# Performance work log

Measured on AMD Instinct MI355X. Metric: run time of the kernel, lower is better.

Reference implementation:

```python
import jax, jax.numpy as jnp
import numpy as np

B, R, K, C, H, E = 256, 6, 49, 512, 1024, 300
NV, NR, NL = 504, 190, 2001


def setup_inputs() -> dict:
    key = jax.random.key(0)
    ks = list(jax.random.split(key, 40))
    it = iter(ks)

    def nrm(shape, s=0.02):
        return jax.random.normal(next(it), shape, jnp.float32) * s

    return dict(
        v_org=jax.random.normal(next(it), (B, C, 7, 7), jnp.float32),
        img_feat=jax.random.normal(next(it), (B, K, C), jnp.float32),
        gt_verb=jax.random.randint(next(it), (B,), 0, NV),
        role_idx=jax.random.randint(next(it), (B, R), 0, NR),
        mask=jnp.ones((B, R, R), jnp.int32),
        verb_table=nrm((NV, E)),
        role_table=nrm((NR, E)),
        qc_W=nrm((2 * E, H)), qc_b=jnp.zeros((H,), jnp.float32),
        av_W=nrm((C, H)), av_b=jnp.zeros((H,), jnp.float32),
        aq_W=nrm((H, H)), aq_b=jnp.zeros((H,), jnp.float32),
        ao_W=nrm((H, 1)), ao_b=jnp.zeros((1,), jnp.float32),
        vn_W=nrm((C, H)), vn_b=jnp.zeros((H,), jnp.float32),
        qn_W=nrm((H, H)), qn_b=jnp.zeros((H,), jnp.float32),
        Wq=nrm((H, H)), Wk=nrm((H, H)), Wv=nrm((H, H)), Wo=nrm((H, H)),
        uqc_W=nrm((H + 2 * E, H)), uqc_b=jnp.zeros((H,), jnp.float32),
        cls_W=nrm((H, NL)), cls_b=jnp.zeros((NL,), jnp.float32),
    )


def _mfb(q_repr, v_repr):
    # elementwise MFB pool (n_heads=1 -> sumpool is identity), sign-sqrt, L2 norm
    z = q_repr * v_repr
    s = jnp.sqrt(jax.nn.relu(z)) - jnp.sqrt(jax.nn.relu(-z))
    n = jnp.sqrt(jnp.sum(s * s, axis=1, keepdims=True))
    return s / jnp.maximum(n, 1e-12)


def _v_att(img, q_emb, av_W, av_b, aq_W, aq_b, ao_W, ao_b):
    v = jax.nn.relu(img @ av_W + av_b)            # [N,K,H]
    q = jax.nn.relu(q_emb @ aq_W + aq_b)          # [N,H]
    logits = (v * q[:, None, :]) @ ao_W + ao_b    # [N,K,1]
    return jax.nn.softmax(logits, axis=1)


def reference(v_org, img_feat, gt_verb, role_idx, mask, verb_table, role_table,
              qc_W, qc_b, av_W, av_b, aq_W, aq_b, ao_W, ao_b,
              vn_W, vn_b, qn_W, qn_b, Wq, Wk, Wv, Wo,
              uqc_W, uqc_b, cls_W, cls_b):
    Bn, Cn, h, w = v_org.shape
    Rn = role_idx.shape[1]
    img0 = v_org.reshape(Bn, Cn, h * w).transpose(0, 2, 1)          # [B,K,C]
    img = jnp.broadcast_to(img0[:, None], (Bn, Rn, h * w, Cn)).reshape(Bn * Rn, h * w, Cn)
    Kv, Cv = img_feat.shape[1], img_feat.shape[2]
    img_v = jnp.broadcast_to(img_feat[:, None], (Bn, Rn, Kv, Cv)).reshape(Bn * Rn, Kv, Cv)

    verb_e = verb_table[gt_verb]                                     # [B,E]
    role_e = role_table[role_idx]                                    # [B,R,E]
    rv = jnp.concatenate([jnp.broadcast_to(verb_e[:, None], (Bn, Rn, verb_e.shape[-1])), role_e], -1)
    rv = rv.reshape(Bn * Rn, -1)                                     # [BR,2E]

    q_emb = jax.nn.relu(rv @ qc_W + qc_b)

    att = _v_att(img, q_emb, av_W, av_b, aq_W, aq_b, ao_W, ao_b)
    v_emb = (att * img).sum(1)
    v_repr = jax.nn.relu(v_emb @ vn_W + vn_b)
    q_repr = jax.nn.relu(q_emb @ qn_W + qn_b)
    out = _mfb(q_repr, v_repr)
    ans0 = out

    att_v = _v_att(img_v, q_emb, av_W, av_b, aq_W, aq_b, ao_W, ao_b)
    v_repr_verb = jax.nn.relu((att_v * img_v).sum(1) @ vn_W + vn_b)
    out_verb = _mfb(q_repr, v_repr_verb)

    # masked neighbour attention over role nodes (single head)
    Hd = out.shape[-1]
    cur = out.reshape(Bn, Rn, Hd)
    qh, kh, vh = cur @ Wq, cur @ Wk, cur @ Wv
    scores = jnp.einsum('bid,bjd->bij', qh, kh) / jnp.sqrt(jnp.float32(Hd))
    m = mask.astype(jnp.float32) * (1.0 - jnp.eye(Rn, dtype=jnp.float32))  # no self edges
    scores = jnp.where(m > 0, scores, jnp.float32(-1e9))
    attn = jax.nn.softmax(scores, axis=-1)
    neigh = (jnp.einsum('bij,bjd->bid', attn, vh) @ Wo).reshape(Bn * Rn, Hd)

    uq = jax.nn.relu(jnp.concatenate([neigh, rv], -1) @ uqc_W + uqc_b)
    att2 = _v_att(img, uq, av_W, av_b, aq_W, aq_b, ao_W, ao_b)
    v_repr2 = jax.nn.relu((att2 * img).sum(1) @ vn_W + vn_b)
    q_repr2 = jax.nn.relu(uq @ qn_W + qn_b)
    out2 = _mfb(q_repr2, v_repr2)

    gate = jax.nn.sigmoid(out2 + out_verb)
    out_f = (1.0 - gate) * out_verb + gate * jnp.tanh(out2 + ans0)

    logits = out_f @ cls_W + cls_b
    return logits.reshape(Bn, Rn, -1)
```

## Files before the change

kernel.cpp:

```cpp
#include <hip/hip_runtime.h>
#include <math.h>

typedef unsigned short u16;
typedef __attribute__((ext_vector_type(8))) short short8;
typedef __attribute__((ext_vector_type(4))) float f32x4;

#define Bb 256
#define Rr 6
#define Ksp 49
#define Cc 512
#define Hh 1024
#define Ee 300
#define NN (Bb*Rr)
#define NLl 2001

__device__ __forceinline__ u16 f2b(float x) {
    union { float f; unsigned u; } c; c.f = x;
    unsigned r = c.u + 0x7fffu + ((c.u >> 16) & 1u);
    return (u16)(r >> 16);
}
__device__ __forceinline__ float b2f(u16 b) {
    union { unsigned u; float f; } c; c.u = ((unsigned)b) << 16; return c.f;
}

#define ASYNC16(gp, lp) __builtin_amdgcn_global_load_lds( \
    (const __attribute__((address_space(1))) unsigned int*)(gp), \
    (__attribute__((address_space(3))) unsigned int*)(lp), 16, 0, 0)

constexpr size_t O_QC   = 0;
constexpr size_t O_AV   = O_QC   + (size_t)1024*640;
constexpr size_t O_AQQN = O_AV   + (size_t)1024*512;
constexpr size_t O_VN   = O_AQQN + (size_t)2048*1024;
constexpr size_t O_QKV  = O_VN   + (size_t)1024*512;
constexpr size_t O_WO   = O_QKV  + (size_t)3072*1024;
constexpr size_t O_UQC  = O_WO   + (size_t)1024*1024;
constexpr size_t O_CLS  = O_UQC  + (size_t)1024*1664;
constexpr size_t WT_ELEMS = O_CLS + (size_t)2048*1024;

template<int BM, int BN, int BK>
__global__ void __launch_bounds__(256) gemm_bf16(
    const u16* __restrict__ A, int lda, const u16* __restrict__ Bt,
    const float* __restrict__ bias,
    u16* __restrict__ Cb, int ldcb, float* __restrict__ Cf, int ldcf,
    int K, int split, int Nreal, int act)
{
    constexpr int SM = BM / 16, SN = BN / 16;
    constexpr int KG = BK / 32;
    constexpr int WM = BM / 32, WN = BN / 32;
    constexpr int BUF = (SM + SN) * KG * 512;
    __shared__ u16 lds[2 * BUF];
    const int tid  = threadIdx.x;
    const int wave = tid >> 6, lane = tid & 63;
    const int m0 = lane & 15, q0 = lane >> 4;

    const int gn = gridDim.x;
    const int nblk = gn * gridDim.y;
    const int lid = blockIdx.y * gn + blockIdx.x;
    const int per = nblk >> 3, rem = nblk & 7;
    const int xcd = lid & 7, slot = lid >> 3;
    const int t = xcd * per + ((xcd < rem) ? xcd : rem) + slot;
    const int tm = t / gn, tn = t - tm * gn;
    const int bm = tm * BM, bn = tn * BN;
    const int wr = wave >> 1, wc = wave & 1;

    auto stage = [&](int kt, int buf) {
        u16* l = &lds[buf * BUF];
        #pragma unroll
        for (int s = wave; s < SM; s += 4)
            #pragma unroll
            for (int g = 0; g < KG; g++) {
                const u16* gp = A + (size_t)(bm + s * 16 + m0) * lda + kt + g * 32 + q0 * 8;
                ASYNC16(gp, &l[(s * KG + g) * 512]);
            }
        #pragma unroll
        for (int s = wave; s < SN; s += 4)
            #pragma unroll
            for (int g = 0; g < KG; g++) {
                const u16* gp = Bt + (size_t)(bn + s * 16 + m0) * K + kt + g * 32 + q0 * 8;
                ASYNC16(gp, &l[(SM * KG + s * KG + g) * 512]);
            }
    };

    f32x4 acc[WM][WN];
    #pragma unroll
    for (int i = 0; i < WM; i++)
        #pragma unroll
        for (int j = 0; j < WN; j++)
            acc[i][j] = (f32x4){0.f, 0.f, 0.f, 0.f};

    stage(0, 0);
    const int nIter = K / BK;
    for (int it = 0; it < nIter; ++it) {
        __syncthreads();
        if (it + 1 < nIter) stage((it + 1) * BK, (it + 1) & 1);
        const u16* l = &lds[(it & 1) * BUF];
        short8 af[WM][KG], bf[WN][KG];
        #pragma unroll
        for (int i = 0; i < WM; i++)
            #pragma unroll
            for (int g = 0; g < KG; g++)
                af[i][g] = *(const short8*)&l[(((wr * WM + i) * KG + g) * 64 + lane) * 8];
        #pragma unroll
        for (int j = 0; j < WN; j++)
            #pragma unroll
            for (int g = 0; g < KG; g++)
                bf[j][g] = *(const short8*)&l[((SM * KG + (wc * WN + j) * KG + g) * 64 + lane) * 8];
        #pragma unroll
        for (int g = 0; g < KG; g++)
            #pragma unroll
            for (int i = 0; i < WM; i++)
                #pragma unroll
                for (int j = 0; j < WN; j++)
                    acc[i][j] = __builtin_amdgcn_mfma_f32_16x16x32_bf16(
                        af[i][g], bf[j][g], acc[i][j], 0, 0, 0);
    }

    #pragma unroll
    for (int i = 0; i < WM; i++) {
        #pragma unroll
        for (int j = 0; j < WN; j++) {
            const int col = bn + (wc * WN + j) * 16 + m0;
            if (col >= Nreal) continue;
            const float bv = bias ? bias[col] : 0.f;
            #pragma unroll
            for (int r = 0; r < 4; r++) {
                const int row = bm + (wr * WM + i) * 16 + q0 * 4 + r;
                float v = acc[i][j][r] + bv;
                if (act) v = fmaxf(v, 0.f);
                if (col < split) Cb[(size_t)row * ldcb + col] = f2b(v);
                else             Cf[(size_t)row * ldcf + col - split] = v;
            }
        }
    }
}

struct PrepSrc { const float* s[11]; };

__global__ void __launch_bounds__(256) prep_kernel(
    PrepSrc ps, u16* __restrict__ wt,
    const float* __restrict__ verb_table, const float* __restrict__ role_table,
    const int* __restrict__ gt_verb, const int* __restrict__ role_idx,
    u16* __restrict__ cat,
    const float* __restrict__ v_org, u16* __restrict__ A1,
    const float* __restrict__ img_feat, u16* __restrict__ A2,
    const float* __restrict__ aq_b, const float* __restrict__ qn_b,
    float* __restrict__ aqqn_b)
{
    __shared__ float sm[64 * 50];
    const int bid = blockIdx.x, tid = threadIdx.x;

    if (bid < 11520) {
        const int tStart[12] = {0,640,1152,2176,3200,3712,4736,5760,6784,7808,9472,11520};
        const int tK[11]  = {600,512,1024,1024,512,1024,1024,1024,1024,1624,1024};
        const int tN[11]  = {1024,1024,1024,1024,1024,1024,1024,1024,1024,1024,2001};
        const int tKp[11] = {640,512,1024,1024,512,1024,1024,1024,1024,1664,1024};
        const int tNp[11] = {1024,1024,1024,1024,1024,1024,1024,1024,1024,1024,2048};
        const long tDst[11] = {(long)O_QC,(long)O_AV,(long)O_AQQN,(long)(O_AQQN+1048576),
                               (long)O_VN,(long)O_QKV,(long)(O_QKV+1048576),
                               (long)(O_QKV+2097152),(long)O_WO,(long)O_UQC,(long)O_CLS};
        int e = 0;
        while (bid >= tStart[e + 1]) e++;
        const int local = bid - tStart[e];
        const int ktiles = tKp[e] >> 5;
        const int bx = local % ktiles, by = local / ktiles;
        const float* W = ps.s[e];
        u16* Wt = wt + tDst[e];
        const int K = tK[e], Nn = tN[e], Kp = tKp[e], Np = tNp[e];
        const int kt = bx * 32, nt = by * 32;
        const int tx = tid & 31, ty = tid >> 5;
        for (int i = ty; i < 32; i += 8) {
            const int k = kt + i, n = nt + tx;
            sm[i * 33 + tx] = (k < K && n < Nn) ? W[(size_t)k * Nn + n] : 0.f;
        }
        __syncthreads();
        for (int i = ty; i < 32; i += 8) {
            const int n = nt + i, k = kt + tx;
            if (n < Np && k < Kp) Wt[(size_t)n * Kp + k] = f2b(sm[tx * 33 + i]);
        }
    } else if (bid < 15360) {
        const int idx = (bid - 11520) * 256 + tid;
        const int n = idx / 640;
        const int col = idx - n * 640;
        const int b = n / Rr, r = n - b * Rr;
        float v = 0.f;
        if (col < Ee)          v = verb_table[(size_t)gt_verb[b] * Ee + col];
        else if (col < 2 * Ee) v = role_table[(size_t)role_idx[b * Rr + r] * Ee + (col - Ee)];
        cat[(size_t)n * 1664 + 1024 + col] = f2b(v);
    } else if (bid < 17408) {
        const int local = bid - 15360;
        const int b = local >> 3, c0 = (local & 7) << 6;
        {
            const int ci = tid >> 2, k0 = tid & 3;
            const float* p = v_org + ((size_t)b * Cc + c0 + ci) * Ksp;
            for (int k = k0; k < Ksp; k += 4) sm[ci * 50 + k] = p[k];
        }
        __syncthreads();
        {
            const int cc = tid & 63, kb = tid >> 6;
            for (int k = kb; k < Ksp; k += 4)
                A1[((size_t)b * Ksp + k) * Cc + c0 + cc] = f2b(sm[cc * 50 + k]);
        }
    } else if (bid < 23680) {
        const int i = (bid - 17408) * 256 + tid;
        const float4 v = ((const float4*)img_feat)[i];
        ushort4 o;
        o.x = f2b(v.x); o.y = f2b(v.y); o.z = f2b(v.z); o.w = f2b(v.w);
        ((ushort4*)A2)[i] = o;
    } else {
        const int i = (bid - 23680) * 256 + tid;
        if (i < 2048) aqqn_b[i] = (i < 1024) ? aq_b[i] : qn_b[i - 1024];
    }
}

__global__ void __launch_bounds__(256) att_kernel(
    const u16* __restrict__ Vh0,
    const u16* __restrict__ Q,
    const float* __restrict__ aoW, const float* __restrict__ aoB,
    const u16* __restrict__ IMG0,
    u16* __restrict__ Vemb0)
{
    const int task = blockIdx.x >> 8;
    const int b = blockIdx.x & 255;
    const u16* Vh   = Vh0   + (size_t)task * 12544 * 1024;
    const u16* IMGb = IMG0  + (size_t)task * 12544 * 512;
    u16* Vemb       = Vemb0 + (size_t)task * NN * 512;
    const int tid = threadIdx.x, wave = tid >> 6, lane = tid & 63;
    __shared__ u16 s_qs[16][1032];
    __shared__ float s_log[64][6];
    __shared__ float s_att[49][6];

    for (int n = 0; n < 16; n++) {
        const u16* qp = Q + ((size_t)b * Rr + n) * Hh;
        for (int h = tid; h < 1032; h += 256) {
            u16 v = 0;
            if (n < Rr && h < Hh) v = f2b(b2f(qp[h]) * aoW[h]);
            s_qs[n][h] = v;
        }
    }
    __syncthreads();

    const int m = lane & 15, q = lane >> 4;
    {
        f32x4 acc = (f32x4){0.f, 0.f, 0.f, 0.f};
        const u16* arow = Vh + ((size_t)b * Ksp + wave * 16 + m) * Hh + q * 8;
        const u16* brow = &s_qs[m][q * 8];
        for (int kt = 0; kt < Hh; kt += 32) {
            const short8 af = *(const short8*)(arow + kt);
            const short8 bf = *(const short8*)(brow + kt);
            acc = __builtin_amdgcn_mfma_f32_16x16x32_bf16(af, bf, acc, 0, 0, 0);
        }
        const float aob = aoB[0];
        #pragma unroll
        for (int r = 0; r < 4; r++) {
            const int k = wave * 16 + q * 4 + r;
            if (k < Ksp && m < Rr) s_log[k][m] = acc[r] + aob;
        }
    }
    __syncthreads();

    if (wave == 0) {
        for (int r = 0; r < Rr; r++) {
            const float v = (lane < Ksp) ? s_log[lane][r] : -INFINITY;
            float mx = v;
            #pragma unroll
            for (int off = 32; off; off >>= 1) mx = fmaxf(mx, __shfl_down(mx, off));
            mx = __shfl(mx, 0);
            const float e = (lane < Ksp) ? expf(v - mx) : 0.f;
            float s = e;
            #pragma unroll
            for (int off = 32; off; off >>= 1) s += __shfl_down(s, off);
            s = __shfl(s, 0);
            if (lane < Ksp) s_att[lane][r] = e / s;
        }
    }
    __syncthreads();

    float acc2[Rr][2];
    #pragma unroll
    for (int r = 0; r < Rr; r++) { acc2[r][0] = 0.f; acc2[r][1] = 0.f; }
    const u16* ib = IMGb + (size_t)b * Ksp * Cc + tid * 2;
    #pragma unroll 7
    for (int k = 0; k < Ksp; k++) {
        const ushort2 v = *(const ushort2*)(ib + (size_t)k * Cc);
        const float v0 = b2f(v.x), v1 = b2f(v.y);
        #pragma unroll
        for (int r = 0; r < Rr; r++) {
            const float w = s_att[k][r];
            acc2[r][0] += w * v0; acc2[r][1] += w * v1;
        }
    }
    #pragma unroll
    for (int r = 0; r < Rr; r++) {
        ushort2 o; o.x = f2b(acc2[r][0]); o.y = f2b(acc2[r][1]);
        *(ushort2*)(Vemb + ((size_t)b * Rr + r) * Cc + tid * 2) = o;
    }
}

__global__ void __launch_bounds__(256) mfb2_kernel(
    const float* __restrict__ q, const float* __restrict__ v,
    float* __restrict__ a0f, u16* __restrict__ a0b, float* __restrict__ vbf)
{
    const int n = blockIdx.x;
    const int qrow = (n < NN) ? n : n - NN;
    const int tid = threadIdx.x;
    __shared__ float red[4];
    float sv[4];
    float local = 0.f;
    #pragma unroll
    for (int i = 0; i < 4; i++) {
        const int h = tid + i * 256;
        const float z = q[(size_t)qrow * Hh + h] * v[(size_t)n * Hh + h];
        const float s = (z > 0.f) ? sqrtf(z) : -sqrtf(-z);
        sv[i] = s;
        local += s * s;
    }
    #pragma unroll
    for (int off = 32; off; off >>= 1) local += __shfl_down(local, off);
    if ((tid & 63) == 0) red[tid >> 6] = local;
    __syncthreads();
    const float tot = red[0] + red[1] + red[2] + red[3];
    const float inv = 1.f / fmaxf(sqrtf(tot), 1e-12f);
    #pragma unroll
    for (int i = 0; i < 4; i++) {
        const float o = sv[i] * inv;
        if (n < NN) {
            const size_t off2 = (size_t)n * Hh + tid + i * 256;
            a0f[off2] = o; a0b[off2] = f2b(o);
        } else {
            vbf[(size_t)(n - NN) * Hh + tid + i * 256] = o;
        }
    }
}

__global__ void __launch_bounds__(256) mfb_gate_kernel(
    const float* __restrict__ q, const float* __restrict__ v,
    const float* __restrict__ ovb, const float* __restrict__ oa0,
    u16* __restrict__ outb)
{
    const int n = blockIdx.x;
    const int tid = threadIdx.x;
    __shared__ float red[4];
    float sv[4];
    float local = 0.f;
    #pragma unroll
    for (int i = 0; i < 4; i++) {
        const int h = tid + i * 256;
        const float z = q[(size_t)n * Hh + h] * v[(size_t)n * Hh + h];
        const float s = (z > 0.f) ? sqrtf(z) : -sqrtf(-z);
        sv[i] = s;
        local += s * s;
    }
    #pragma unroll
    for (int off = 32; off; off >>= 1) local += __shfl_down(local, off);
    if ((tid & 63) == 0) red[tid >> 6] = local;
    __syncthreads();
    const float tot = red[0] + red[1] + red[2] + red[3];
    const float inv = 1.f / fmaxf(sqrtf(tot), 1e-12f);
    #pragma unroll
    for (int i = 0; i < 4; i++) {
        const size_t off2 = (size_t)n * Hh + tid + i * 256;
        const float o2 = sv[i] * inv;
        const float ov = ovb[off2], a0 = oa0[off2];
        const float g = 1.f / (1.f + expf(-(o2 + ov)));
        outb[off2] = f2b((1.f - g) * ov + g * tanhf(o2 + a0));
    }
}

__global__ void __launch_bounds__(256) nattn_kernel(
    const u16* __restrict__ qkv, const int* __restrict__ mask,
    u16* __restrict__ nv)
{
    const int b = blockIdx.x;
    const int tid = threadIdx.x;
    __shared__ float s_sc[Rr][Rr];
    __shared__ float s_at[Rr][Rr];
    const int wave = tid >> 6, lane = tid & 63;
    for (int p = wave; p < Rr * Rr; p += 4) {
        const int i = p / Rr, j = p - (p / Rr) * Rr;
        const u16* qp = qkv + ((size_t)(b * Rr + i)) * 3072;
        const u16* kp = qkv + ((size_t)(b * Rr + j)) * 3072 + 1024;
        float s = 0.f;
        for (int h = lane * 2; h < Hh; h += 128) {
            const ushort2 qv = *(const ushort2*)(qp + h);
            const ushort2 kv = *(const ushort2*)(kp + h);
            s += b2f(qv.x) * b2f(kv.x) + b2f(qv.y) * b2f(kv.y);
        }
        #pragma unroll
        for (int off = 32; off; off >>= 1) s += __shfl_down(s, off);
        if (lane == 0) s_sc[i][j] = s * 0.03125f;
    }
    __syncthreads();
    if (tid < Rr) {
        const int i = tid;
        float vals[Rr];
        float m = -INFINITY;
        #pragma unroll
        for (int j = 0; j < Rr; j++) {
            const float mij = (i == j) ? 0.f : (float)mask[b * Rr * Rr + i * Rr + j];
            const float v = (mij > 0.f) ? s_sc[i][j] : -1e9f;
            vals[j] = v;
            m = fmaxf(m, v);
        }
        float ssum = 0.f;
        #pragma unroll
        for (int j = 0; j < Rr; j++) { const float e = expf(vals[j] - m); s_at[i][j] = e; ssum += e; }
        const float invs = 1.f / ssum;
        #pragma unroll
        for (int j = 0; j < Rr; j++) s_at[i][j] *= invs;
    }
    __syncthreads();
    for (int h = tid; h < Hh; h += 256) {
        #pragma unroll
        for (int i = 0; i < Rr; i++) {
            float acc = 0.f;
            #pragma unroll
            for (int j = 0; j < Rr; j++)
                acc += s_at[i][j] * b2f(qkv[((size_t)(b * Rr + j)) * 3072 + 2048 + h]);
            nv[((size_t)(b * Rr + i)) * Hh + h] = f2b(acc);
        }
    }
}

extern "C" void kernel_launch(void* const* d_in, const int* in_sizes, int n_in,
                              void* d_out, int out_size, void* d_ws, size_t ws_size,
                              hipStream_t stream)
{
    const float* v_org      = (const float*)d_in[0];
    const float* img_feat   = (const float*)d_in[1];
    const int*   gt_verb    = (const int*)d_in[2];
    const int*   role_idx   = (const int*)d_in[3];
    const int*   mask       = (const int*)d_in[4];
    const float* verb_table = (const float*)d_in[5];
    const float* role_table = (const float*)d_in[6];
    const float* qc_W  = (const float*)d_in[7];
    const float* qc_b  = (const float*)d_in[8];
    const float* av_W  = (const float*)d_in[9];
    const float* av_b  = (const float*)d_in[10];
    const float* aq_W  = (const float*)d_in[11];
    const float* aq_b  = (const float*)d_in[12];
    const float* ao_W  = (const float*)d_in[13];
    const float* ao_b  = (const float*)d_in[14];
    const float* vn_W  = (const float*)d_in[15];
    const float* vn_b  = (const float*)d_in[16];
    const float* qn_W  = (const float*)d_in[17];
    const float* qn_b  = (const float*)d_in[18];
    const float* Wq    = (const float*)d_in[19];
    const float* Wk    = (const float*)d_in[20];
    const float* Wv    = (const float*)d_in[21];
    const float* Wo    = (const float*)d_in[22];
    const float* uqc_W = (const float*)d_in[23];
    const float* uqc_b = (const float*)d_in[24];
    const float* cls_W = (const float*)d_in[25];
    const float* cls_b = (const float*)d_in[26];
    float* out = (float*)d_out;

    char* base = (char*)d_ws;
    size_t off = 0;
    auto alloc = [&](size_t bytes) -> char* {
        char* p = base + off;
        off += (bytes + 255) & ~(size_t)255;
        return p;
    };
    u16* wt = (u16*)alloc(WT_ELEMS * 2);
    u16* A1 = (u16*)alloc((size_t)12544 * 512 * 2 * 2);
    u16* A2 = A1 + (size_t)12544 * 512;
    u16* v_img = (u16*)alloc((size_t)12544 * 1024 * 2 * 2);
    u16* v_imgv = v_img + (size_t)12544 * 1024;
    u16* qkv = (u16*)v_imgv;
    u16* nv  = (u16*)((char*)v_imgv + (size_t)NN * 3072 * 2);
    u16* cat    = (u16*)alloc((size_t)NN * 1664 * 2);
    u16* q_emb  = (u16*)alloc((size_t)NN * 1024 * 2);
    u16* q_att  = (u16*)alloc((size_t)NN * 1024 * 2);
    u16* uq     = (u16*)alloc((size_t)NN * 1024 * 2);
    u16* out_f  = (u16*)alloc((size_t)NN * 1024 * 2);
    u16* v_emb2 = (u16*)alloc((size_t)2 * NN * 512 * 2);
    float* v_rep2 = (float*)alloc((size_t)2 * NN * 1024 * 4);
    float* q_rep = (float*)alloc((size_t)NN * 1024 * 4);
    float* a0f   = (float*)alloc((size_t)NN * 1024 * 4);
    u16*   a0b   = (u16*)alloc((size_t)NN * 1024 * 2);
    float* vbf   = (float*)alloc((size_t)NN * 1024 * 4);
    float* aqqn_b = (float*)alloc(2048 * 4);

    const dim3 blk(256);

    PrepSrc ps;
    ps.s[0] = qc_W;  ps.s[1] = av_W; ps.s[2] = aq_W; ps.s[3] = qn_W;
    ps.s[4] = vn_W;  ps.s[5] = Wq;   ps.s[6] = Wk;   ps.s[7] = Wv;
    ps.s[8] = Wo;    ps.s[9] = uqc_W; ps.s[10] = cls_W;
    prep_kernel<<<dim3(23688), blk, 0, stream>>>(
        ps, wt, verb_table, role_table, gt_verb, role_idx, cat,
        v_org, A1, img_feat, A2, aq_b, qn_b, aqqn_b);

    gemm_bf16<32,64,64><<<dim3(16, 48), blk, 0, stream>>>(
        cat + 1024, 1664, wt + O_QC, qc_b, q_emb, 1024, nullptr, 0,
        640, 1024, 1024, 1);
    gemm_bf16<128,128,32><<<dim3(8, 196), blk, 0, stream>>>(
        A1, 512, wt + O_AV, av_b, v_img, 1024, nullptr, 0,
        512, 1024, 1024, 1);
    gemm_bf16<32,64,64><<<dim3(32, 48), blk, 0, stream>>>(
        q_emb, 1024, wt + O_AQQN, aqqn_b, q_att, 1024, q_rep, 1024,
        1024, 1024, 2048, 1);
    att_kernel<<<dim3(512), blk, 0, stream>>>(v_img, q_att, ao_W, ao_b, A1, v_emb2);
    gemm_bf16<32,64,64><<<dim3(16, 96), blk, 0, stream>>>(
        v_emb2, 512, wt + O_VN, vn_b, nullptr, 0, v_rep2, 1024,
        512, 0, 1024, 1);
    mfb2_kernel<<<dim3(2 * NN), blk, 0, stream>>>(q_rep, v_rep2, a0f, a0b, vbf);
    gemm_bf16<32,64,64><<<dim3(48, 48), blk, 0, stream>>>(
        a0b, 1024, wt + O_QKV, nullptr, qkv, 3072, nullptr, 0,
        1024, 3072, 3072, 0);
    nattn_kernel<<<dim3(Bb), blk, 0, stream>>>(qkv, mask, nv);
    gemm_bf16<32,64,64><<<dim3(16, 48), blk, 0, stream>>>(
        nv, 1024, wt + O_WO, nullptr, cat, 1664, nullptr, 0,
        1024, 1024, 1024, 0);
    gemm_bf16<32,64,64><<<dim3(16, 48), blk, 0, stream>>>(
        cat, 1664, wt + O_UQC, uqc_b, uq, 1024, nullptr, 0,
        1664, 1024, 1024, 1);
    gemm_bf16<32,64,64><<<dim3(32, 48), blk, 0, stream>>>(
        uq, 1024, wt + O_AQQN, aqqn_b, q_att, 1024, q_rep, 1024,
        1024, 1024, 2048, 1);
    att_kernel<<<dim3(Bb), blk, 0, stream>>>(v_img, q_att, ao_W, ao_b, A1, v_emb2);
    gemm_bf16<32,64,64><<<dim3(16, 48), blk, 0, stream>>>(
        v_emb2, 512, wt + O_VN, vn_b, nullptr, 0, v_rep2, 1024,
        512, 0, 1024, 1);
    mfb_gate_kernel<<<dim3(NN), blk, 0, stream>>>(q_rep, v_rep2, vbf, a0f, out_f);
    gemm_bf16<32,64,64><<<dim3(32, 48), blk, 0, stream>>>(
        out_f, 1024, wt + O_CLS, cls_b, nullptr, 0, out, 2001,
        1024, 0, 2001, 0);
}
```

Before: 606.5 us.

## Replace LDS-tiled small GEMMs with direct-global-load MFMA kernel using 64x64 tiles

Adds a GEMM kernel that skips LDS staging and double buffering. Each wave loads its A fragment and four B fragments straight from global memory into registers and issues 16x16x32 bf16 MFMAs, so a block covers a 64x64 output tile. All the medium GEMMs (qc, aq/qn, vn, qkv, Wo, uqc, cls) now use it with grids sized for the larger tile. The aim is to cut LDS traffic, barriers and launch overhead. The cost is no data reuse across waves through shared memory, uncoalesced 16-byte strided loads, and more reliance on the L2/MALL caches.

```diff
diff --git a/kernel.cpp b/kernel.cpp
--- a/kernel.cpp
+++ b/kernel.cpp
@@ -36,6 +36,62 @@
 constexpr size_t O_UQC  = O_WO   + (size_t)1024*1024;
 constexpr size_t O_CLS  = O_UQC  + (size_t)1024*1664;
 constexpr size_t WT_ELEMS = O_CLS + (size_t)2048*1024;
+
+__global__ void __launch_bounds__(256) wgemm_bf16(
+    const u16* __restrict__ A, int lda, const u16* __restrict__ Bt,
+    const float* __restrict__ bias,
+    u16* __restrict__ Cb, int ldcb, float* __restrict__ Cf, int ldcf,
+    int K, int split, int Nreal, int act)
+{
+    const int tid = threadIdx.x, wave = tid >> 6, lane = tid & 63;
+    const int m0 = lane & 15, q0 = lane >> 4;
+
+    const int gn = gridDim.x;
+    const int nblk = gn * gridDim.y;
+    const int lid = blockIdx.y * gn + blockIdx.x;
+    const int per = nblk >> 3, rem = nblk & 7;
+    const int xcd = lid & 7, slot = lid >> 3;
+    const int t = xcd * per + ((xcd < rem) ? xcd : rem) + slot;
+    const int tm = t / gn, tn = t - tm * gn;
+
+    const int bm = tm * 64 + wave * 16;
+    const int bn = tn * 64;
+
+    const u16* arow = A + (size_t)(bm + m0) * lda + q0 * 8;
+    const u16* brow0 = Bt + (size_t)(bn + m0) * K + q0 * 8;
+
+    f32x4 acc[4];
+    #pragma unroll
+    for (int j = 0; j < 4; j++) acc[j] = (f32x4){0.f, 0.f, 0.f, 0.f};
+
+    for (int kt = 0; kt < K; kt += 128) {
+        #pragma unroll
+        for (int u = 0; u < 4; u++) {
+            const int k = kt + u * 32;
+            const short8 av = *(const short8*)(arow + k);
+            #pragma unroll
+            for (int j = 0; j < 4; j++) {
+                const short8 bv = *(const short8*)(brow0 + (size_t)j * 16 * K + k);
+                acc[j] = __builtin_amdgcn_mfma_f32_16x16x32_bf16(av, bv, acc[j], 0, 0, 0);
+            }
+        }
+    }
+
+    #pragma unroll
+    for (int j = 0; j < 4; j++) {
+        const int col = bn + j * 16 + m0;
+        if (col >= Nreal) continue;
+        const float bv = bias ? bias[col] : 0.f;
+        #pragma unroll
+        for (int r = 0; r < 4; r++) {
+            const int row = bm + q0 * 4 + r;
+            float v = acc[j][r] + bv;
+            if (act) v = fmaxf(v, 0.f);
+            if (col < split) Cb[(size_t)row * ldcb + col] = f2b(v);
+            else             Cf[(size_t)row * ldcf + col - split] = v;
+        }
+    }
+}
 
 template<int BM, int BN, int BK>
 __global__ void __launch_bounds__(256) gemm_bf16(
@@ -491,39 +547,39 @@
         ps, wt, verb_table, role_table, gt_verb, role_idx, cat,
         v_org, A1, img_feat, A2, aq_b, qn_b, aqqn_b);
 
-    gemm_bf16<32,64,64><<<dim3(16, 48), blk, 0, stream>>>(
+    wgemm_bf16<<<dim3(16, 24), blk, 0, stream>>>(
         cat + 1024, 1664, wt + O_QC, qc_b, q_emb, 1024, nullptr, 0,
         640, 1024, 1024, 1);
     gemm_bf16<128,128,32><<<dim3(8, 196), blk, 0, stream>>>(
         A1, 512, wt + O_AV, av_b, v_img, 1024, nullptr, 0,
         512, 1024, 1024, 1);
-    gemm_bf16<32,64,64><<<dim3(32, 48), blk, 0, stream>>>(
+    wgemm_bf16<<<dim3(32, 24), blk, 0, stream>>>(
         q_emb, 1024, wt + O_AQQN, aqqn_b, q_att, 1024, q_rep, 1024,
         1024, 1024, 2048, 1);
     att_kernel<<<dim3(512), blk, 0, stream>>>(v_img, q_att, ao_W, ao_b, A1, v_emb2);
-    gemm_bf16<32,64,64><<<dim3(16, 96), blk, 0, stream>>>(
+    wgemm_bf16<<<dim3(16, 48), blk, 0, stream>>>(
         v_emb2, 512, wt + O_VN, vn_b, nullptr, 0, v_rep2, 1024,
         512, 0, 1024, 1);
     mfb2_kernel<<<dim3(2 * NN), blk, 0, stream>>>(q_rep, v_rep2, a0f, a0b, vbf);
-    gemm_bf16<32,64,64><<<dim3(48, 48), blk, 0, stream>>>(
+    wgemm_bf16<<<dim3(48, 24), blk, 0, stream>>>(
         a0b, 1024, wt + O_QKV, nullptr, qkv, 3072, nullptr, 0,
         1024, 3072, 3072, 0);
     nattn_kernel<<<dim3(Bb), blk, 0, stream>>>(qkv, mask, nv);
-    gemm_bf16<32,64,64><<<dim3(16, 48), blk, 0, stream>>>(
+    wgemm_bf16<<<dim3(16, 24), blk, 0, stream>>>(
         nv, 1024, wt + O_WO, nullptr, cat, 1664, nullptr, 0,
         1024, 1024, 1024, 0);
-    gemm_bf16<32,64,64><<<dim3(16, 48), blk, 0, stream>>>(
+    wgemm_bf16<<<dim3(16, 24), blk, 0, stream>>>(
         cat, 1664, wt + O_UQC, uqc_b, uq, 1024, nullptr, 0,
         1664, 1024, 1024, 1);
-    gemm_bf16<32,64,64><<<dim3(32, 48), blk, 0, stream>>>(
+    wgemm_bf16<<<dim3(32, 24), blk, 0, stream>>>(
         uq, 1024, wt + O_AQQN, aqqn_b, q_att, 1024, q_rep, 1024,
         1024, 1024, 2048, 1);
     att_kernel<<<dim3(Bb), blk, 0, stream>>>(v_img, q_att, ao_W, ao_b, A1, v_emb2);
-    gemm_bf16<32,64,64><<<dim3(16, 48), blk, 0, stream>>>(
+    wgemm_bf16<<<dim3(16, 24), blk, 0, stream>>>(
         v_emb2, 512, wt + O_VN, vn_b, nullptr, 0, v_rep2, 1024,
         512, 0, 1024, 1);
     mfb_gate_kernel<<<dim3(NN), blk, 0, stream>>>(q_rep, v_rep2, vbf, a0f, out_f);
-    gemm_bf16<32,64,64><<<dim3(32, 48), blk, 0, stream>>>(
+    wgemm_bf16<<<dim3(32, 24), blk, 0, stream>>>(
         out_f, 1024, wt + O_CLS, cls_b, nullptr, 0, out, 2001,
         1024, 0, 2001, 0);
 }
```

Result: slower. 791.4 us (+30.5%).
